# Kernel optimization log

Hardware: AMD Instinct MI355X
Metric: run time of the kernel (lower is better)

Reference implementation:

```python
import jax, jax.numpy as jnp
import numpy as np

B, T, C, H = 4, 2048, 1024, 16
INIT_STD = 0.02

def setup_inputs() -> dict:
    key = jax.random.key(0)
    ks = jax.random.split(key, 9)
    x = jax.random.normal(ks[0], (B, T, C), dtype=jnp.float32)
    def dense(kw):
        return jax.random.normal(kw, (C, C), dtype=jnp.float32) * INIT_STD
    return {
        "x": x,
        "Wq": dense(ks[1]), "bq": jnp.zeros((C,), jnp.float32),
        "Wk": dense(ks[2]), "bk": jnp.zeros((C,), jnp.float32),
        "Wv": dense(ks[3]), "bv": jnp.zeros((C,), jnp.float32),
        "Wo": dense(ks[4]), "bo": jnp.zeros((C,), jnp.float32),
    }

def reference(x, Wq, bq, Wk, bk, Wv, bv, Wo, bo):
    b, t, c = x.shape
    hd = c // H  # head dim
    # QKV projections, reshape to (B, H, T, hd)
    def split_heads(y):
        return jnp.transpose(y.reshape(b, t, H, hd), (0, 2, 1, 3))
    q = split_heads(x @ Wq + bq)
    k = split_heads(x @ Wk + bk)
    v = split_heads(x @ Wv + bv)
    scale = 1.0 / jnp.sqrt(jnp.float32(hd))
    att = jnp.einsum('bhqd,bhkd->bhqk', q, k) * scale  # [B,H,T,T]
    mask = jnp.tril(jnp.ones((t, t), dtype=bool))[None, None]
    att = jnp.where(mask, att, jnp.float32(-jnp.inf))
    att = jax.nn.softmax(att, axis=-1)
    y = jnp.einsum('bhqk,bhkd->bhqd', att, v)  # [B,H,T,hd]
    y = jnp.transpose(y, (0, 2, 1, 3)).reshape(b, t, c)
    return y @ Wo + bo
```

## Files before the change

kernel.cpp:

```cpp
#include <hip/hip_runtime.h>
#include <hip/hip_bf16.h>
#include <stdint.h>

typedef __bf16 bf16;
typedef __attribute__((ext_vector_type(8))) __bf16 bf16x8;
typedef __attribute__((ext_vector_type(4))) __bf16 bf16x4;
typedef __attribute__((ext_vector_type(4))) float f32x4;

constexpr int Bn = 4, Tn = 2048, Cn = 1024, Hn = 16, HD = 64;
constexpr int Mn = Bn * Tn;

__device__ __forceinline__ void gl_lds16(const void* g, void* l) {
  __builtin_amdgcn_global_load_lds(
      (const __attribute__((address_space(1))) void*)g,
      (__attribute__((address_space(3))) void*)l, 16u, 0, 0u);
}

__global__ __launch_bounds__(256) void k_cvt_x(const float* __restrict__ x,
                                               bf16* __restrict__ xb) {
  int i = (blockIdx.x * 256 + threadIdx.x) * 8;
  float4 a = *(const float4*)(x + i);
  float4 b = *(const float4*)(x + i + 4);
  bf16x8 v;
  v[0] = (bf16)a.x; v[1] = (bf16)a.y; v[2] = (bf16)a.z; v[3] = (bf16)a.w;
  v[4] = (bf16)b.x; v[5] = (bf16)b.y; v[6] = (bf16)b.z; v[7] = (bf16)b.w;
  *(bf16x8*)(xb + i) = v;
}

__global__ __launch_bounds__(256) void k_tw(const float* __restrict__ W0,
                                            const float* __restrict__ W1,
                                            const float* __restrict__ W2,
                                            const float* __restrict__ W3,
                                            bf16* __restrict__ WT) {
  __shared__ float tile[32][33];
  const float* W = (blockIdx.z == 0) ? W0 : (blockIdx.z == 1) ? W1
                  : (blockIdx.z == 2) ? W2 : W3;
  bf16* out = WT + (size_t)blockIdx.z * Cn * Cn;
  int tx = threadIdx.x & 31, ty = threadIdx.x >> 5;
  int gx = blockIdx.x * 32 + tx;
  int gy = blockIdx.y * 32;
#pragma unroll
  for (int j = 0; j < 32; j += 8)
    tile[ty + j][tx] = W[(size_t)(gy + ty + j) * Cn + gx];
  __syncthreads();
  int ox = blockIdx.y * 32 + tx;
  int oy = blockIdx.x * 32;
#pragma unroll
  for (int j = 0; j < 32; j += 8)
    out[(size_t)(oy + ty + j) * Cn + ox] = (bf16)tile[tx][ty + j];
}

#define GEMM_CORE(ACC)                                                      \
  const int t = threadIdx.x, l = t & 63, w = t >> 6;                        \
  const int g = l >> 4, q16 = l & 15;                                       \
  const int wm = w >> 2, wn = w & 3;                                        \
  const int xm = (q16 & 7) << 4;                                            \
  const int qkB0 = q16 * 128 + ((g * 16) ^ xm);                             \
  const int qkB1 = q16 * 128 + ((64 + g * 16) ^ xm);                        \
  const int srow = t >> 3;                                                  \
  const int sseg = (t & 7) ^ (srow & 7);                                    \
  const bf16* aP0 = A + (size_t)(m0 + srow) * 1024 + sseg * 8;              \
  const bf16* aP1 = aP0 + 65536;                                            \
  const bf16* bP0 = BT + (size_t)(n0 + srow) * 1024 + sseg * 8;             \
  const bf16* bP1 = bP0 + 65536;                                            \
  f32x4 ACC[4][2] = {};                                                     \
                                            \
  gl_lds16(aP0, sm + w * 1024);                                             \
  gl_lds16(aP1, sm + 8192 + w * 1024);                                      \
  gl_lds16(bP0, sm + 16384 + w * 1024);                                     \
  gl_lds16(bP1, sm + 24576 + w * 1024);                                     \
  _Pragma("unroll")                                                         \
  for (int j = 0; j < 16; ++j) {                                            \
    const int BK_ = (j & 1) ? 32768 : 0;                                    \
    const int NB_ = 32768 - BK_;                                            \
    const bool more = j < 15;                                               \
    if (more) {                                                             \
      gl_lds16(aP0 + (j + 1) * 64, sm + NB_ + w * 1024);                    \
      gl_lds16(aP1 + (j + 1) * 64, sm + NB_ + 8192 + w * 1024);             \
      gl_lds16(bP0 + (j + 1) * 64, sm + NB_ + 16384 + w * 1024);            \
      gl_lds16(bP1 + (j + 1) * 64, sm + NB_ + 24576 + w * 1024);            \
      asm volatile("s_waitcnt vmcnt(4)" ::: "memory");                      \
    } else {                                                                \
      asm volatile("s_waitcnt vmcnt(0)" ::: "memory");                      \
    }                                                                       \
    __builtin_amdgcn_sched_barrier(0);                                      \
    __builtin_amdgcn_s_barrier();                                           \
    bf16x8 bfr[2][2], af0[2], af1[2];                                       \
    _Pragma("unroll") for (int ni = 0; ni < 2; ++ni) {                      \
      bfr[ni][0] = *(const bf16x8*)(sm + BK_ + 16384 + wn * 4096 +          \
                                    ni * 2048 + qkB0);                      \
      bfr[ni][1] = *(const bf16x8*)(sm + BK_ + 16384 + wn * 4096 +          \
                                    ni * 2048 + qkB1);                      \
    }                                                                       \
    af0[0] = *(const bf16x8*)(sm + BK_ + wm * 8192 + qkB0);                 \
    af0[1] = *(const bf16x8*)(sm + BK_ + wm * 8192 + qkB1);                 \
    af1[0] = *(const bf16x8*)(sm + BK_ + wm * 8192 + 2048 + qkB0);          \
    af1[1] = *(const bf16x8*)(sm + BK_ + wm * 8192 + 2048 + qkB1);          \
    __builtin_amdgcn_s_setprio(1);                                          \
    _Pragma("unroll") for (int ni = 0; ni < 2; ++ni) {                      \
      ACC[0][ni] = __builtin_amdgcn_mfma_f32_16x16x32_bf16(                 \
          af0[0], bfr[ni][0], ACC[0][ni], 0, 0, 0);                         \
      ACC[0][ni] = __builtin_amdgcn_mfma_f32_16x16x32_bf16(                 \
          af0[1], bfr[ni][1], ACC[0][ni], 0, 0, 0);                         \
      ACC[1][ni] = __builtin_amdgcn_mfma_f32_16x16x32_bf16(                 \
          af1[0], bfr[ni][0], ACC[1][ni], 0, 0, 0);                         \
      ACC[1][ni] = __builtin_amdgcn_mfma_f32_16x16x32_bf16(                 \
          af1[1], bfr[ni][1], ACC[1][ni], 0, 0, 0);                         \
    }                                                                       \
    __builtin_amdgcn_s_setprio(0);                                          \
    af0[0] = *(const bf16x8*)(sm + BK_ + wm * 8192 + 4096 + qkB0);          \
    af0[1] = *(const bf16x8*)(sm + BK_ + wm * 8192 + 4096 + qkB1);          \
    af1[0] = *(const bf16x8*)(sm + BK_ + wm * 8192 + 6144 + qkB0);          \
    af1[1] = *(const bf16x8*)(sm + BK_ + wm * 8192 + 6144 + qkB1);          \
    __builtin_amdgcn_s_setprio(1);                                          \
    _Pragma("unroll") for (int ni = 0; ni < 2; ++ni) {                      \
      ACC[2][ni] = __builtin_amdgcn_mfma_f32_16x16x32_bf16(                 \
          af0[0], bfr[ni][0], ACC[2][ni], 0, 0, 0);                         \
      ACC[2][ni] = __builtin_amdgcn_mfma_f32_16x16x32_bf16(                 \
          af0[1], bfr[ni][1], ACC[2][ni], 0, 0, 0);                         \
      ACC[3][ni] = __builtin_amdgcn_mfma_f32_16x16x32_bf16(                 \
          af1[0], bfr[ni][0], ACC[3][ni], 0, 0, 0);                         \
      ACC[3][ni] = __builtin_amdgcn_mfma_f32_16x16x32_bf16(                 \
          af1[1], bfr[ni][1], ACC[3][ni], 0, 0, 0);                         \
    }                                                                       \
    __builtin_amdgcn_s_setprio(0);                                          \
    __builtin_amdgcn_s_barrier();                                           \
  }

__global__ __launch_bounds__(512, 2) void k_gemm_qkv8(
    const bf16* __restrict__ A, const bf16* __restrict__ BT,
    const float* __restrict__ bq, const float* __restrict__ bk,
    const float* __restrict__ bv, bf16* __restrict__ out, float qscale) {
  __shared__ __align__(16) char sm[65536];
  const int b0 = blockIdx.x;
  const int blk = (b0 & 7) * 192 + (b0 >> 3);
  const int m0 = (blk / 24) * 128, n0 = (blk % 24) * 128;
  GEMM_CORE(acc)
#pragma unroll
  for (int ni = 0; ni < 2; ++ni) {
    int colBase = n0 + wn * 32 + ni * 16;
    int which = colBase >> 10;
    const float* bp = (which == 0) ? bq : (which == 1) ? bk : bv;
    float scl = (which == 0) ? qscale : 1.0f;
    float bval = bp[(colBase & 1023) + q16];
    int hh = (colBase >> 6) & 15;
    int dd = (colBase & 63) + q16;
    size_t obase = (size_t)which * 8388608 + (size_t)hh * (Tn * HD) + dd;
#pragma unroll
    for (int mi = 0; mi < 4; ++mi) {
#pragma unroll
      for (int r = 0; r < 4; ++r) {
        int row = m0 + wm * 64 + mi * 16 + g * 4 + r;
        int bb = row >> 11, tt = row & 2047;
        out[obase + ((size_t)bb * Hn * Tn + tt) * HD] =
            (bf16)((acc[mi][ni][r] + bval) * scl);
      }
    }
  }
}

__global__ __launch_bounds__(512, 2) void k_gemm_o8(
    const bf16* __restrict__ A, const bf16* __restrict__ BT,
    const float* __restrict__ bias, float* __restrict__ out) {
  __shared__ __align__(16) char sm[65536];
  const int b0 = blockIdx.x;
  const int blk = (b0 & 7) * 64 + (b0 >> 3);
  const int m0 = (blk >> 3) * 128, n0 = (blk & 7) * 128;
  GEMM_CORE(acc)
#pragma unroll
  for (int ni = 0; ni < 2; ++ni) {
    int col = n0 + wn * 32 + ni * 16 + q16;
    float bv = bias[col];
#pragma unroll
    for (int mi = 0; mi < 4; ++mi) {
#pragma unroll
      for (int r = 0; r < 4; ++r) {
        int row = m0 + wm * 64 + mi * 16 + g * 4 + r;
        out[(size_t)row * Cn + col] = acc[mi][ni][r] + bv;
      }
    }
  }
}

__global__ __launch_bounds__(512, 4) void k_attn(const bf16* __restrict__ Q,
                                                 const bf16* __restrict__ K,
                                                 const bf16* __restrict__ V,
                                                 bf16* __restrict__ Y) {
  __shared__ __align__(16) char smem[32768];
  const int t = threadIdx.x, w = t >> 6, l = t & 63;
  const int g = l >> 4, q16 = l & 15;
  const int wg = blockIdx.x;
  const int bh = wg & 63;
  const int qtile = 15 - (wg >> 6);
  const size_t base = (size_t)bh * Tn * HD;
  const bf16* Qh = Q + base;
  const bf16* Vh = V + base;
  const int qg = qtile * 128 + w * 16 + q16;

  bf16x8 aq[2];
#pragma unroll
  for (int kc = 0; kc < 2; ++kc)
    aq[kc] = *(const bf16x8*)(Qh + (size_t)qg * HD + kc * 32 + g * 8);

  const int xm = (q16 & 7) << 4;
  const int qkB0 = q16 * 128 + ((g * 16) ^ xm);
  const int qkB1 = q16 * 128 + ((64 + g * 16) ^ xm);
  const int innerL = (l >> 5) * 64 + ((l & 15) >> 2) * 16 +
                     (((l >> 4) & 1) * 4 + (l & 3)) * 2;
  int stb[8];
#pragma unroll
  for (int j = 0; j < 8; ++j)
    stb[j] = w * 1024 + j * 128 + (innerL ^ (j << 4));

  const int krow = w * 8 + (l >> 3);
  const int kseg = (l & 7) ^ (krow & 7);
  const bf16* kP = K + base + (size_t)krow * HD + kseg * 8;
  const bf16* vP = Vh + (size_t)l * HD + w * 8;

  f32x4 yacc[4] = {};
  float m_ = -1e30f, l_ = 0.f;
  const int nt = 2 * qtile + 2;
  const int it_mask = 2 * qtile + (w >= 4 ? 1 : 0);
  const int diag = (w & 3) * 16 + q16;

#define STAGE_K(KBUF)                           \
  {                                             \
    gl_lds16(kP, smem + (KBUF) + w * 1024);     \
    kP += 4096;                                 \
  }
#define WRITE_V(VBUF, a0)                               \
  {                                                     \
    _Pragma("unroll") for (int j = 0; j < 8; ++j)       \
      *(bf16*)(smem + (VBUF) + stb[j]) = a0[j];         \
  }
#define COMPUTE(KBUF, VBUF, DOMASK)                                          \
  {                                                                          \
    f32x4 s[4] = {};                                                         \
    __builtin_amdgcn_s_setprio(1);                                           \
    _Pragma("unroll") for (int nj = 0; nj < 4; ++nj) {                       \
      bf16x8 ak0 = *(const bf16x8*)(smem + (KBUF) + qkB0 + nj * 2048);       \
      s[nj] = __builtin_amdgcn_mfma_f32_16x16x32_bf16(ak0, aq[0], s[nj], 0, 0, 0); \
      bf16x8 ak1 = *(const bf16x8*)(smem + (KBUF) + qkB1 + nj * 2048);       \
      s[nj] = __builtin_amdgcn_mfma_f32_16x16x32_bf16(ak1, aq[1], s[nj], 0, 0, 0); \
    }                                                                        \
    __builtin_amdgcn_s_setprio(0);                                           \
    if (DOMASK) {                                                            \
      _Pragma("unroll") for (int nj = 0; nj < 4; ++nj)                       \
        _Pragma("unroll") for (int r = 0; r < 4; ++r)                        \
          if (nj * 16 + g * 4 + r > diag) s[nj][r] = -1e30f;                 \
    }                                                                        \
    float mx = fmaxf(fmaxf(fmaxf(s[0][0], s[0][1]), fmaxf(s[0][2], s[0][3])),\
                     fmaxf(fmaxf(s[1][0], s[1][1]), fmaxf(s[1][2], s[1][3])));\
    mx = fmaxf(mx, fmaxf(fmaxf(fmaxf(s[2][0], s[2][1]), fmaxf(s[2][2], s[2][3])),\
                         fmaxf(fmaxf(s[3][0], s[3][1]), fmaxf(s[3][2], s[3][3]))));\
    mx = fmaxf(mx, __shfl_xor(mx, 16));                                      \
    mx = fmaxf(mx, __shfl_xor(mx, 32));                                      \
    float mn = fmaxf(m_, mx);                                                \
    float fac = __builtin_amdgcn_exp2f(m_ - mn);                             \
    m_ = mn;                                                                 \
    float rs = 0.f;                                                          \
    _Pragma("unroll") for (int nj = 0; nj < 4; ++nj)                         \
      _Pragma("unroll") for (int r = 0; r < 4; ++r) {                        \
        float pv = __builtin_amdgcn_exp2f(s[nj][r] - mn);                    \
        s[nj][r] = pv;                                                       \
        rs += pv;                                                            \
      }                                                                      \
    rs += __shfl_xor(rs, 16);                                                \
    rs += __shfl_xor(rs, 32);                                                \
    l_ = l_ * fac + rs;                                                      \
    _Pragma("unroll") for (int ni = 0; ni < 4; ++ni)                         \
      _Pragma("unroll") for (int r = 0; r < 4; ++r) yacc[ni][r] *= fac;      \
    __builtin_amdgcn_s_setprio(1);                                           \
    _Pragma("unroll") for (int vkc = 0; vkc < 2; ++vkc) {                    \
      bf16x8 pb;                                                             \
      _Pragma("unroll") for (int j = 0; j < 4; ++j) {                        \
        pb[j] = (bf16)s[2 * vkc][j];                                         \
        pb[4 + j] = (bf16)s[2 * vkc + 1][j];                                 \
      }                                                                      \
      int vb = (vkc == 0) ? qkB0 : qkB1;                                     \
      _Pragma("unroll") for (int ni = 0; ni < 4; ++ni) {                     \
        bf16x8 va = *(const bf16x8*)(smem + (VBUF) + vb + ni * 2048);        \
        yacc[ni] = __builtin_amdgcn_mfma_f32_16x16x32_bf16(va, pb, yacc[ni], 0, 0, 0); \
      }                                                                      \
    }                                                                        \
    __builtin_amdgcn_s_setprio(0);                                           \
  }

  STAGE_K(0);
  {
    bf16x8 a0 = *(const bf16x8*)vP;
    vP += 4096;
    WRITE_V(16384, a0);
  }

  int it = 0;
  for (;;) {
    __syncthreads();
    bool more = (it + 1) < nt;
    bf16x8 a0;
    if (more) {
      STAGE_K(8192);
      a0 = *(const bf16x8*)vP;
      vP += 4096;
    }
    if (it <= it_mask) COMPUTE(0, 16384, it == it_mask);
    if (more) WRITE_V(24576, a0);
    if (++it >= nt) break;

    __syncthreads();
    more = (it + 1) < nt;
    if (more) {
      STAGE_K(0);
      a0 = *(const bf16x8*)vP;
      vP += 4096;
    }
    if (it <= it_mask) COMPUTE(8192, 24576, it == it_mask);
    if (more) WRITE_V(16384, a0);
    if (++it >= nt) break;
  }
#undef STAGE_K
#undef WRITE_V
#undef COMPUTE

  const int hh = bh & 15, bb = bh >> 4;
  float inv = 1.f / l_;
#pragma unroll
  for (int ni = 0; ni < 4; ++ni) {
    bf16x4 o;
#pragma unroll
    for (int r = 0; r < 4; ++r) o[r] = (bf16)(yacc[ni][r] * inv);
    int d0 = ni * 16 + g * 4;
    *(bf16x4*)&Y[(size_t)(bb * Tn + qg) * Cn + hh * HD + d0] = o;
  }
}

extern "C" void kernel_launch(void* const* d_in, const int* in_sizes, int n_in,
                              void* d_out, int out_size, void* d_ws,
                              size_t ws_size, hipStream_t stream) {
  const float* x  = (const float*)d_in[0];
  const float* Wq = (const float*)d_in[1];
  const float* bq = (const float*)d_in[2];
  const float* Wk = (const float*)d_in[3];
  const float* bk = (const float*)d_in[4];
  const float* Wv = (const float*)d_in[5];
  const float* bv = (const float*)d_in[6];
  const float* Wo = (const float*)d_in[7];
  const float* bo = (const float*)d_in[8];
  char* ws = (char*)d_ws;
  bf16* xb = (bf16*)ws;
  bf16* WT = (bf16*)(ws + (size_t)(16 << 20));
  bf16* Qh = (bf16*)(ws + (size_t)(24 << 20));
  bf16* Kh = (bf16*)(ws + (size_t)(40 << 20));
  bf16* Vh = (bf16*)(ws + (size_t)(56 << 20));
  float* out = (float*)d_out;

  const float QSCALE = 0.125f * 1.44269504088896f;

  k_cvt_x<<<4096, 256, 0, stream>>>(x, xb);
  k_tw<<<dim3(32, 32, 4), 256, 0, stream>>>(Wq, Wk, Wv, Wo, WT);
  k_gemm_qkv8<<<1536, 512, 0, stream>>>(xb, WT, bq, bk, bv, Qh, QSCALE);
  k_attn<<<1024, 512, 0, stream>>>(Qh, Kh, Vh, xb);
  k_gemm_o8<<<512, 512, 0, stream>>>(xb, WT + (3u << 20), bo, out);
}
```

Before: 152.0 us.

## Split K across wave groups in GEMM core with LDS reduction

The GEMM core changes from eight waves each owning a 64x32 output slice to two groups of four waves. Each group takes one half of every 64-wide K step and owns a 64x64 output slice with a 4x4 accumulator grid. This cuts the LDS fragment loads per MFMA, since each wave now reads 8 fragments for 16 MFMAs instead of 12 for 16. The cost is double the accumulator registers (64 floats), a final LDS reduction pass with an extra __syncthreads, and only half the waves doing the epilogue stores.

```diff
diff --git a/kernel.cpp b/kernel.cpp
--- a/kernel.cpp
+++ b/kernel.cpp
@@ -50,21 +50,19 @@
     out[(size_t)(oy + ty + j) * Cn + ox] = (bf16)tile[tx][ty + j];
 }
 
-#define GEMM_CORE(ACC)                                                      \
+#define GEMM_CORE_KS(ACC)                                                   \
   const int t = threadIdx.x, l = t & 63, w = t >> 6;                        \
   const int g = l >> 4, q16 = l & 15;                                       \
-  const int wm = w >> 2, wn = w & 3;                                        \
+  const int kc = w >> 2, wm = (w >> 1) & 1, wn = w & 1;                     \
   const int xm = (q16 & 7) << 4;                                            \
-  const int qkB0 = q16 * 128 + ((g * 16) ^ xm);                             \
-  const int qkB1 = q16 * 128 + ((64 + g * 16) ^ xm);                        \
+  const int qkB = q16 * 128 + ((kc * 64 + g * 16) ^ xm);                    \
   const int srow = t >> 3;                                                  \
   const int sseg = (t & 7) ^ (srow & 7);                                    \
   const bf16* aP0 = A + (size_t)(m0 + srow) * 1024 + sseg * 8;              \
   const bf16* aP1 = aP0 + 65536;                                            \
   const bf16* bP0 = BT + (size_t)(n0 + srow) * 1024 + sseg * 8;             \
   const bf16* bP1 = bP0 + 65536;                                            \
-  f32x4 ACC[4][2] = {};                                                     \
-                                            \
+  f32x4 ACC[4][4] = {};                                                     \
   gl_lds16(aP0, sm + w * 1024);                                             \
   gl_lds16(aP1, sm + 8192 + w * 1024);                                      \
   gl_lds16(bP0, sm + 16384 + w * 1024);                                     \
@@ -85,46 +83,36 @@
     }                                                                       \
     __builtin_amdgcn_sched_barrier(0);                                      \
     __builtin_amdgcn_s_barrier();                                           \
-    bf16x8 bfr[2][2], af0[2], af1[2];                                       \
-    _Pragma("unroll") for (int ni = 0; ni < 2; ++ni) {                      \
-      bfr[ni][0] = *(const bf16x8*)(sm + BK_ + 16384 + wn * 4096 +          \
-                                    ni * 2048 + qkB0);                      \
-      bfr[ni][1] = *(const bf16x8*)(sm + BK_ + 16384 + wn * 4096 +          \
-                                    ni * 2048 + qkB1);                      \
-    }                                                                       \
-    af0[0] = *(const bf16x8*)(sm + BK_ + wm * 8192 + qkB0);                 \
-    af0[1] = *(const bf16x8*)(sm + BK_ + wm * 8192 + qkB1);                 \
-    af1[0] = *(const bf16x8*)(sm + BK_ + wm * 8192 + 2048 + qkB0);          \
-    af1[1] = *(const bf16x8*)(sm + BK_ + wm * 8192 + 2048 + qkB1);          \
+    bf16x8 af[4], bfv[4];                                                   \
+    _Pragma("unroll") for (int mi = 0; mi < 4; ++mi)                        \
+      af[mi] = *(const bf16x8*)(sm + BK_ + wm * 8192 + mi * 2048 + qkB);    \
+    _Pragma("unroll") for (int ni = 0; ni < 4; ++ni)                        \
+      bfv[ni] = *(const bf16x8*)(sm + BK_ + 16384 + wn * 8192 +             \
+                                 ni * 2048 + qkB);                          \
     __builtin_amdgcn_s_setprio(1);                                          \
-    _Pragma("unroll") for (int ni = 0; ni < 2; ++ni) {                      \
-      ACC[0][ni] = __builtin_amdgcn_mfma_f32_16x16x32_bf16(                 \
-          af0[0], bfr[ni][0], ACC[0][ni], 0, 0, 0);                         \
-      ACC[0][ni] = __builtin_amdgcn_mfma_f32_16x16x32_bf16(                 \
-          af0[1], bfr[ni][1], ACC[0][ni], 0, 0, 0);                         \
-      ACC[1][ni] = __builtin_amdgcn_mfma_f32_16x16x32_bf16(                 \
-          af1[0], bfr[ni][0], ACC[1][ni], 0, 0, 0);                         \
-      ACC[1][ni] = __builtin_amdgcn_mfma_f32_16x16x32_bf16(                 \
-          af1[1], bfr[ni][1], ACC[1][ni], 0, 0, 0);                         \
-    }                                                                       \
-    __builtin_amdgcn_s_setprio(0);                                          \
-    af0[0] = *(const bf16x8*)(sm + BK_ + wm * 8192 + 4096 + qkB0);          \
-    af0[1] = *(const bf16x8*)(sm + BK_ + wm * 8192 + 4096 + qkB1);          \
-    af1[0] = *(const bf16x8*)(sm + BK_ + wm * 8192 + 6144 + qkB0);          \
-    af1[1] = *(const bf16x8*)(sm + BK_ + wm * 8192 + 6144 + qkB1);          \
-    __builtin_amdgcn_s_setprio(1);                                          \
-    _Pragma("unroll") for (int ni = 0; ni < 2; ++ni) {                      \
-      ACC[2][ni] = __builtin_amdgcn_mfma_f32_16x16x32_bf16(                 \
-          af0[0], bfr[ni][0], ACC[2][ni], 0, 0, 0);                         \
-      ACC[2][ni] = __builtin_amdgcn_mfma_f32_16x16x32_bf16(                 \
-          af0[1], bfr[ni][1], ACC[2][ni], 0, 0, 0);                         \
-      ACC[3][ni] = __builtin_amdgcn_mfma_f32_16x16x32_bf16(                 \
-          af1[0], bfr[ni][0], ACC[3][ni], 0, 0, 0);                         \
-      ACC[3][ni] = __builtin_amdgcn_mfma_f32_16x16x32_bf16(                 \
-          af1[1], bfr[ni][1], ACC[3][ni], 0, 0, 0);                         \
-    }                                                                       \
+    _Pragma("unroll") for (int mi = 0; mi < 4; ++mi)                        \
+      _Pragma("unroll") for (int ni = 0; ni < 4; ++ni)                      \
+        ACC[mi][ni] = __builtin_amdgcn_mfma_f32_16x16x32_bf16(              \
+            af[mi], bfv[ni], ACC[mi][ni], 0, 0, 0);                         \
     __builtin_amdgcn_s_setprio(0);                                          \
     __builtin_amdgcn_s_barrier();                                           \
+  }                                                                         \
+               \
+  if (w >= 4) {                                                             \
+    _Pragma("unroll") for (int mi = 0; mi < 4; ++mi)                        \
+      _Pragma("unroll") for (int ni = 0; ni < 4; ++ni)                      \
+        *(f32x4*)(sm + (w - 4) * 16384 + (mi * 4 + ni) * 1024 + l * 16) =   \
+            ACC[mi][ni];                                                    \
+  }                                                                         \
+  __syncthreads();                                                          \
+  if (w < 4) {                                                              \
+    _Pragma("unroll") for (int mi = 0; mi < 4; ++mi)                        \
+      _Pragma("unroll") for (int ni = 0; ni < 4; ++ni) {                    \
+        f32x4 p = *(const f32x4*)(sm + w * 16384 + (mi * 4 + ni) * 1024 +   \
+                                  l * 16);                                  \
+        _Pragma("unroll") for (int r = 0; r < 4; ++r)                       \
+          ACC[mi][ni][r] += p[r];                                           \
+      }                                                                     \
   }
 
 __global__ __launch_bounds__(512, 2) void k_gemm_qkv8(
@@ -135,25 +123,27 @@
   const int b0 = blockIdx.x;
   const int blk = (b0 & 7) * 192 + (b0 >> 3);
   const int m0 = (blk / 24) * 128, n0 = (blk % 24) * 128;
-  GEMM_CORE(acc)
-#pragma unroll
-  for (int ni = 0; ni < 2; ++ni) {
-    int colBase = n0 + wn * 32 + ni * 16;
-    int which = colBase >> 10;
-    const float* bp = (which == 0) ? bq : (which == 1) ? bk : bv;
-    float scl = (which == 0) ? qscale : 1.0f;
-    float bval = bp[(colBase & 1023) + q16];
-    int hh = (colBase >> 6) & 15;
-    int dd = (colBase & 63) + q16;
-    size_t obase = (size_t)which * 8388608 + (size_t)hh * (Tn * HD) + dd;
-#pragma unroll
-    for (int mi = 0; mi < 4; ++mi) {
-#pragma unroll
-      for (int r = 0; r < 4; ++r) {
-        int row = m0 + wm * 64 + mi * 16 + g * 4 + r;
-        int bb = row >> 11, tt = row & 2047;
-        out[obase + ((size_t)bb * Hn * Tn + tt) * HD] =
-            (bf16)((acc[mi][ni][r] + bval) * scl);
+  GEMM_CORE_KS(acc)
+  if (w < 4) {
+#pragma unroll
+    for (int ni = 0; ni < 4; ++ni) {
+      int colBase = n0 + wn * 64 + ni * 16;
+      int which = colBase >> 10;
+      const float* bp = (which == 0) ? bq : (which == 1) ? bk : bv;
+      float scl = (which == 0) ? qscale : 1.0f;
+      float bval = bp[(colBase & 1023) + q16];
+      int hh = (colBase >> 6) & 15;
+      int dd = (colBase & 63) + q16;
+      size_t obase = (size_t)which * 8388608 + (size_t)hh * (Tn * HD) + dd;
+#pragma unroll
+      for (int mi = 0; mi < 4; ++mi) {
+#pragma unroll
+        for (int r = 0; r < 4; ++r) {
+          int row = m0 + wm * 64 + mi * 16 + g * 4 + r;
+          int bb = row >> 11, tt = row & 2047;
+          out[obase + ((size_t)bb * Hn * Tn + tt) * HD] =
+              (bf16)((acc[mi][ni][r] + bval) * scl);
+        }
       }
     }
   }
@@ -166,17 +156,19 @@
   const int b0 = blockIdx.x;
   const int blk = (b0 & 7) * 64 + (b0 >> 3);
   const int m0 = (blk >> 3) * 128, n0 = (blk & 7) * 128;
-  GEMM_CORE(acc)
-#pragma unroll
-  for (int ni = 0; ni < 2; ++ni) {
-    int col = n0 + wn * 32 + ni * 16 + q16;
-    float bv = bias[col];
-#pragma unroll
-    for (int mi = 0; mi < 4; ++mi) {
-#pragma unroll
-      for (int r = 0; r < 4; ++r) {
-        int row = m0 + wm * 64 + mi * 16 + g * 4 + r;
-        out[(size_t)row * Cn + col] = acc[mi][ni][r] + bv;
+  GEMM_CORE_KS(acc)
+  if (w < 4) {
+#pragma unroll
+    for (int ni = 0; ni < 4; ++ni) {
+      int col = n0 + wn * 64 + ni * 16 + q16;
+      float bv = bias[col];
+#pragma unroll
+      for (int mi = 0; mi < 4; ++mi) {
+#pragma unroll
+        for (int r = 0; r < 4; ++r) {
+          int row = m0 + wm * 64 + mi * 16 + g * 4 + r;
+          out[(size_t)row * Cn + col] = acc[mi][ni][r] + bv;
+        }
       }
     }
   }
```

Result: slower. 160.2 us (+5.4%).
